# Optimization experiments

Measured on AMD Instinct MI355X. Metric: run time of the kernel, lower is better.

## Reference

```python
import jax, jax.numpy as jnp
import numpy as np

DIM = 128; HEADS = 8; HD = DIM // HEADS; RES = 32
HSP, WSP, SSP = 32, 4, 4  # idx=0 cross-shaped window
WIN = HSP * WSP * SSP
SCALE = HD ** -0.5


def setup_inputs() -> dict:
    key = jax.random.key(0)
    k1, k2, k3 = jax.random.split(key, 3)
    qkv = jax.random.normal(k1, (3, 2, RES ** 3, DIM), dtype=jnp.float32)
    w = jax.random.normal(k2, (DIM, 1, 5, 5, 5), dtype=jnp.float32) * 0.05
    b = jax.random.normal(k3, (DIM,), dtype=jnp.float32) * 0.05
    return {"qkv": qkv, "w": w, "b": b}


def _windows(x):
    B = x.shape[0]
    x = x.reshape(B, RES // HSP, HSP, RES // WSP, WSP, RES // SSP, SSP, DIM)
    x = x.transpose(0, 1, 3, 5, 2, 4, 6, 7)
    return x.reshape(-1, WIN, DIM)


def reference(qkv, w, b):
    q, k, v = qkv[0], qkv[1], qkv[2]  # each [B, L, C]
    B = q.shape[0]
    qw = _windows(q).reshape(-1, WIN, HEADS, HD).transpose(0, 2, 1, 3)
    kw = _windows(k).reshape(-1, WIN, HEADS, HD).transpose(0, 2, 1, 3)
    # v windows as [Bw, C, Hsp, Wsp, Ssp] for depthwise LePE conv
    vw = _windows(v).reshape(-1, HSP, WSP, SSP, DIM).transpose(0, 4, 1, 2, 3)
    lepe = jax.lax.conv_general_dilated(
        vw, w, (1, 1, 1), [(2, 2), (2, 2), (2, 2)],
        dimension_numbers=("NCDHW", "OIDHW", "NCDHW"),
        feature_group_count=DIM,
    ) + b[None, :, None, None, None]
    lepe = lepe.reshape(-1, HEADS, HD, WIN).transpose(0, 1, 3, 2)
    vh = vw.reshape(-1, HEADS, HD, WIN).transpose(0, 1, 3, 2)
    attn = jax.nn.softmax(jnp.einsum("bhqd,bhkd->bhqk", qw * SCALE, kw), axis=-1)
    x = jnp.einsum("bhqk,bhkd->bhqd", attn, vh) + lepe
    x = x.transpose(0, 2, 1, 3).reshape(-1, WIN, DIM)
    # windows2img
    x = x.reshape(B, RES // HSP, RES // WSP, RES // SSP, HSP, WSP, SSP, DIM)
    x = x.transpose(0, 1, 4, 2, 5, 3, 6, 7).reshape(B, RES ** 3, DIM)
    return x
```

## Files before the change

kernel.cpp:

```cpp
#include <hip/hip_runtime.h>
#include <stdint.h>

#define DIMC  128
#define HEADS 8
#define HD    16
#define WIN   512
#define LTOT  32768
#define NB    2

typedef __bf16 bf16x8_t __attribute__((ext_vector_type(8)));
typedef float f32x16_t  __attribute__((ext_vector_type(16)));
typedef float f32x4_t   __attribute__((ext_vector_type(4)));
typedef unsigned int u32x2_t __attribute__((ext_vector_type(2)));
union U128 { uint4 u; bf16x8_t v; };

__device__ __forceinline__ uint32_t rne_pair(float lo, float hi) {
    uint32_t a = __float_as_uint(lo), b = __float_as_uint(hi);
    a = (a + 0x7fffu + ((a >> 16) & 1u)) >> 16;
    b = (b + 0x7fffu + ((b >> 16) & 1u)) >> 16;
    return a | (b << 16);
}
__device__ __forceinline__ unsigned short rne1(float x) {
    uint32_t a = __float_as_uint(x);
    return (unsigned short)((a + 0x7fffu + ((a >> 16) & 1u)) >> 16);
}
__device__ __forceinline__ uint32_t trunc_pair(float lo, float hi) {
    return __builtin_amdgcn_perm(__float_as_uint(hi), __float_as_uint(lo), 0x07060302u);
}
__device__ __forceinline__ float fast_exp2(float x) {
#if __has_builtin(__builtin_amdgcn_exp2f)
    return __builtin_amdgcn_exp2f(x);
#else
    return exp2f(x);
#endif
}

__global__ void __launch_bounds__(256, 4) attn_lepe(
    const float* __restrict__ qkv,
    const float* __restrict__ wgt,
    const float* __restrict__ bias,
    float* __restrict__ out)
{
    __shared__ __align__(16) unsigned short Kf[16 * 512];
    __shared__ __align__(16) unsigned short Vt[17 * 520];
    __shared__ __align__(16) unsigned short Wb[125 * 16];
    __shared__ __align__(16) unsigned short Zp[16];

    const int blk  = blockIdx.x;
    const int head = blk >> 7;
    const int wi   = blk & 127;
    const int b    = wi >> 6;
    const int rem  = wi & 63;
    const int lbase = ((rem >> 3) << 7) + ((rem & 7) << 2);
    const int t    = threadIdx.x;
    const int lane = t & 63;
    const int wv   = t >> 6;
    const int cbase = head * HD;

    const int col  = lane & 31;
    const int hsel = lane >> 5;

    const float* Qg = qkv + (size_t)b * LTOT * DIMC;
    const float* Kg = Qg + (size_t)NB * LTOT * DIMC;
    const float* Vg = Kg + (size_t)NB * LTOT * DIMC;

    for (int u = t; u < 1024; u += 256) {
        int tp = u >> 2, ch4 = u & 3;
        int p  = tp << 1;
        int hh = p >> 4, ww = (p >> 2) & 3, ss = p & 3;
        int l  = (hh << 10) + lbase + (ww << 5) + ss;
        size_t g = (size_t)l * DIMC + cbase + (ch4 << 2);
        float4 k0 = *(const float4*)&Kg[g];
        float4 k1 = *(const float4*)&Kg[g + DIMC];
        float4 v0 = *(const float4*)&Vg[g];
        float4 v1 = *(const float4*)&Vg[g + DIMC];
        int c  = p >> 5;
        int fl = (p & 31) + ((ch4 >> 1) << 5);
        int jo = (ch4 & 1) << 2;
        *(uint2*)&Kf[c * 512 + fl * 8 + jo] =
            make_uint2(rne_pair(k0.x, k0.y), rne_pair(k0.z, k0.w));
        *(uint2*)&Kf[c * 512 + (fl + 1) * 8 + jo] =
            make_uint2(rne_pair(k1.x, k1.y), rne_pair(k1.z, k1.w));
        float a0[4] = {v0.x, v0.y, v0.z, v0.w};
        float a1[4] = {v1.x, v1.y, v1.z, v1.w};
#pragma unroll
        for (int i = 0; i < 4; ++i)
            *(uint32_t*)&Vt[((ch4 << 2) + i) * 520 + p] = rne_pair(a0[i], a1[i]);
    }
    if (t < 128) ((uint2*)&Vt[16 * 520])[t] = make_uint2(0x3F803F80u, 0x3F803F80u);
    if (t < 8)  ((uint32_t*)Zp)[t & 7] = 0u;
    for (int e = t; e < 125 * HD; e += 256) {
        int tap = e >> 4, d = e & 15;
        Wb[e] = rne1(wgt[(size_t)(cbase + d) * 125 + tap]);
    }

    const float QSC = 0.25f * 1.44269504088896340736f;
    bf16x8_t qf[4];
#pragma unroll
    for (int mt = 0; mt < 4; ++mt) {
        int qrow = wv * 128 + mt * 32 + col;
        int l = ((qrow >> 4) << 10) + lbase + (((qrow >> 2) & 3) << 5) + (qrow & 3);
        const float* qp = &Qg[(size_t)l * DIMC + cbase + hsel * 8];
        float4 a = *(const float4*)qp;
        float4 c4 = *(const float4*)(qp + 4);
        U128 u;
        u.u.x = rne_pair(a.x * QSC, a.y * QSC);
        u.u.y = rne_pair(a.z * QSC, a.w * QSC);
        u.u.z = rne_pair(c4.x * QSC, c4.y * QSC);
        u.u.w = rne_pair(c4.z * QSC, c4.w * QSC);
        qf[mt] = u.v;
    }
    float breg = (col < HD) ? bias[cbase + col] : 0.f;

    __syncthreads();

    f32x16_t acc[4];
#pragma unroll
    for (int mt = 0; mt < 4; ++mt)
#pragma unroll
        for (int i = 0; i < 16; ++i) acc[mt][i] = 0.f;
    f32x16_t zv;
#pragma unroll
    for (int i = 0; i < 16; ++i) zv[i] = 0.f;

    const int vcol = (col <= 16) ? col : 16;
    const int voff = vcol * 520;

    for (int c = 0; c < 16; ++c) {
        U128 kf;  kf.u  = *(const uint4*)&Kf[c * 512 + lane * 8];
        U128 vf0; vf0.u = *(const uint4*)&Vt[voff + c * 32 + hsel * 8];
        U128 vf1; vf1.u = *(const uint4*)&Vt[voff + c * 32 + 16 + hsel * 8];
#pragma unroll
        for (int mt = 0; mt < 4; ++mt) {
            f32x16_t S = __builtin_amdgcn_mfma_f32_32x32x16_bf16(kf.v, qf[mt], zv, 0, 0, 0);
            uint32_t pk[8];
#pragma unroll
            for (int r = 0; r < 8; ++r)
                pk[r] = trunc_pair(fast_exp2(S[2 * r]), fast_exp2(S[2 * r + 1]));
            U128 A0, A1;
#if __has_builtin(__builtin_amdgcn_permlane32_swap)
            u32x2_t rxz0 = __builtin_amdgcn_permlane32_swap(pk[0], pk[2], false, false);
            u32x2_t ryw0 = __builtin_amdgcn_permlane32_swap(pk[1], pk[3], false, false);
            u32x2_t rxz1 = __builtin_amdgcn_permlane32_swap(pk[4], pk[6], false, false);
            u32x2_t ryw1 = __builtin_amdgcn_permlane32_swap(pk[5], pk[7], false, false);
            A0.u = make_uint4(rxz0[0], ryw0[0], rxz0[1], ryw0[1]);
            A1.u = make_uint4(rxz1[0], ryw1[0], rxz1[1], ryw1[1]);
#else
            uint32_t xa = __shfl_xor(hsel ? pk[0] : pk[2], 32);
            uint32_t xb = __shfl_xor(hsel ? pk[1] : pk[3], 32);
            uint32_t xc = __shfl_xor(hsel ? pk[4] : pk[6], 32);
            uint32_t xd = __shfl_xor(hsel ? pk[5] : pk[7], 32);
            A0.u = hsel ? make_uint4(xa, xb, pk[2], pk[3])
                        : make_uint4(pk[0], pk[1], xa, xb);
            A1.u = hsel ? make_uint4(xc, xd, pk[6], pk[7])
                        : make_uint4(pk[4], pk[5], xc, xd);
#endif
            acc[mt] = __builtin_amdgcn_mfma_f32_32x32x16_bf16(A0.v, vf0.v, acc[mt], 0, 0, 0);
            acc[mt] = __builtin_amdgcn_mfma_f32_32x32x16_bf16(A1.v, vf1.v, acc[mt], 0, 0, 0);
        }
    }

    __syncthreads();

    {
        const int sg  = lane & 15;
        const int khi = lane >> 4;
        const int tb  = (khi & 1) * 8;
#pragma unroll
        for (int cc = 0; cc < 4; ++cc) {
            const int cch = wv * 4 + cc;
            U128 Bf[3];
#pragma unroll
            for (int kc = 0; kc < 3; ++kc) {
                int dh = 2 * kc + (khi >> 1);
                uint32_t pr[4];
#pragma unroll
                for (int jp = 0; jp < 4; ++jp) {
                    uint32_t w01 = 0;
#pragma unroll
                    for (int e = 0; e < 2; ++e) {
                        int tau = tb + jp * 2 + e;
                        int dw = (tau >> 2) - (sg >> 2);
                        int ds = (tau & 3) - (sg & 3);
                        bool valid = (dh < 5) && (dw >= -2) && (dw <= 2) && (ds >= -2) && (ds <= 2);
                        int tap = dh * 25 + (dw + 2) * 5 + (ds + 2);
                        uint32_t wv16 = valid ? (uint32_t)Wb[(valid ? tap : 0) * 16 + cch] : 0u;
                        w01 |= wv16 << (16 * e);
                    }
                    pr[jp] = w01;
                }
                Bf[kc].u = make_uint4(pr[0], pr[1], pr[2], pr[3]);
            }
#pragma unroll
            for (int mt2 = 0; mt2 < 2; ++mt2) {
                f32x4_t cacc = {0.f, 0.f, 0.f, 0.f};
#pragma unroll
                for (int kc = 0; kc < 3; ++kc) {
                    int dh = 2 * kc + (khi >> 1);
                    int h_in = mt2 * 16 + (lane & 15) + dh - 2;
                    const unsigned short* ap =
                        (h_in >= 0 && h_in < 32 && dh < 5)
                            ? &Vt[cch * 520 + h_in * 16 + tb]
                            : Zp;
                    U128 af; af.u = *(const uint4*)ap;
                    cacc = __builtin_amdgcn_mfma_f32_16x16x32_bf16(af.v, Bf[kc].v, cacc, 0, 0, 0);
                }
#pragma unroll
                for (int r = 0; r < 4; ++r) {
                    int h = mt2 * 16 + khi * 4 + r;
                    Kf[(h * 16 + sg) * 16 + cch] = rne1(cacc[r]);
                }
            }
        }
    }

    __syncthreads();

    const int ccol = col & 15;
#pragma unroll
    for (int mt = 0; mt < 4; ++mt) {
#pragma unroll
        for (int i = 0; i < 16; ++i) {
            float dv = __shfl(acc[mt][i], 16 | (lane & 32), 64);
            int row = (i & 3) + ((i >> 2) << 3) + (hsel << 2);
            int token = wv * 128 + mt * 32 + row;
            float cvv = __uint_as_float(((uint32_t)Kf[token * 16 + ccol]) << 16);
            float oval = acc[mt][i] * __builtin_amdgcn_rcpf(dv) + breg + cvv;
            if (col < HD) {
                int l = ((token >> 4) << 10) + lbase + (((token >> 2) & 3) << 5) + (token & 3);
                out[((size_t)b * LTOT + l) * DIMC + cbase + col] = oval;
            }
        }
    }
}

extern "C" void kernel_launch(void* const* d_in, const int* in_sizes, int n_in,
                              void* d_out, int out_size, void* d_ws, size_t ws_size,
                              hipStream_t stream) {
    const float* qkv  = (const float*)d_in[0];
    const float* wgt  = (const float*)d_in[1];
    const float* bias = (const float*)d_in[2];
    float* out = (float*)d_out;
    attn_lepe<<<dim3(1024), dim3(256), 0, stream>>>(qkv, wgt, bias, out);
}
```

Measured before the change: 195.8 us.

## Restructure attention loop into batched QK/exp phase then PV MFMA phase

The inner loop is reordered so each query tile first computes eight key-chunk score MFMAs and their exp/bf16 packing into a register array, then issues the sixteen PV MFMAs back to back under raised wave priority. This is meant to decouple the exp VALU work from dependent MFMA chains and let the scheduler overlap them across waves. Launch bounds drop from 4 to 2 blocks per CU to allow the larger register footprint, which lowers occupancy. It also reloads K and V fragments per query tile instead of once per chunk, adding LDS traffic.

After: 193.8 us. No clear change (-1.0%).

```diff
diff --git a/kernel.cpp b/kernel.cpp
--- a/kernel.cpp
+++ b/kernel.cpp
@@ -35,7 +35,7 @@
 #endif
 }
 
-__global__ void __launch_bounds__(256, 4) attn_lepe(
+__global__ void __launch_bounds__(256, 2) attn_lepe(
     const float* __restrict__ qkv,
     const float* __restrict__ wgt,
     const float* __restrict__ bias,
@@ -126,37 +126,57 @@
     const int vcol = (col <= 16) ? col : 16;
     const int voff = vcol * 520;
 
-    for (int c = 0; c < 16; ++c) {
-        U128 kf;  kf.u  = *(const uint4*)&Kf[c * 512 + lane * 8];
-        U128 vf0; vf0.u = *(const uint4*)&Vt[voff + c * 32 + hsel * 8];
-        U128 vf1; vf1.u = *(const uint4*)&Vt[voff + c * 32 + 16 + hsel * 8];
-#pragma unroll
-        for (int mt = 0; mt < 4; ++mt) {
-            f32x16_t S = __builtin_amdgcn_mfma_f32_32x32x16_bf16(kf.v, qf[mt], zv, 0, 0, 0);
-            uint32_t pk[8];
-#pragma unroll
-            for (int r = 0; r < 8; ++r)
-                pk[r] = trunc_pair(fast_exp2(S[2 * r]), fast_exp2(S[2 * r + 1]));
-            U128 A0, A1;
+#pragma unroll
+    for (int mt = 0; mt < 4; ++mt) {
+#pragma unroll
+        for (int half = 0; half < 2; ++half) {
+            uint32_t pa[8][8];
+
+#pragma unroll
+            for (int cc = 0; cc < 8; ++cc) {
+                const int c = half * 8 + cc;
+                U128 kf; kf.u = *(const uint4*)&Kf[c * 512 + lane * 8];
+                f32x16_t S = __builtin_amdgcn_mfma_f32_32x32x16_bf16(kf.v, qf[mt], zv, 0, 0, 0);
+                float pe[16];
+#pragma unroll
+                for (int r = 0; r < 16; ++r) pe[r] = fast_exp2(S[r]);
+                uint32_t pk[8];
+#pragma unroll
+                for (int r = 0; r < 8; ++r) pk[r] = trunc_pair(pe[2 * r], pe[2 * r + 1]);
 #if __has_builtin(__builtin_amdgcn_permlane32_swap)
-            u32x2_t rxz0 = __builtin_amdgcn_permlane32_swap(pk[0], pk[2], false, false);
-            u32x2_t ryw0 = __builtin_amdgcn_permlane32_swap(pk[1], pk[3], false, false);
-            u32x2_t rxz1 = __builtin_amdgcn_permlane32_swap(pk[4], pk[6], false, false);
-            u32x2_t ryw1 = __builtin_amdgcn_permlane32_swap(pk[5], pk[7], false, false);
-            A0.u = make_uint4(rxz0[0], ryw0[0], rxz0[1], ryw0[1]);
-            A1.u = make_uint4(rxz1[0], ryw1[0], rxz1[1], ryw1[1]);
+                u32x2_t rxz0 = __builtin_amdgcn_permlane32_swap(pk[0], pk[2], false, false);
+                u32x2_t ryw0 = __builtin_amdgcn_permlane32_swap(pk[1], pk[3], false, false);
+                u32x2_t rxz1 = __builtin_amdgcn_permlane32_swap(pk[4], pk[6], false, false);
+                u32x2_t ryw1 = __builtin_amdgcn_permlane32_swap(pk[5], pk[7], false, false);
+                pa[cc][0] = rxz0[0]; pa[cc][1] = ryw0[0];
+                pa[cc][2] = rxz0[1]; pa[cc][3] = ryw0[1];
+                pa[cc][4] = rxz1[0]; pa[cc][5] = ryw1[0];
+                pa[cc][6] = rxz1[1]; pa[cc][7] = ryw1[1];
 #else
-            uint32_t xa = __shfl_xor(hsel ? pk[0] : pk[2], 32);
-            uint32_t xb = __shfl_xor(hsel ? pk[1] : pk[3], 32);
-            uint32_t xc = __shfl_xor(hsel ? pk[4] : pk[6], 32);
-            uint32_t xd = __shfl_xor(hsel ? pk[5] : pk[7], 32);
-            A0.u = hsel ? make_uint4(xa, xb, pk[2], pk[3])
-                        : make_uint4(pk[0], pk[1], xa, xb);
-            A1.u = hsel ? make_uint4(xc, xd, pk[6], pk[7])
-                        : make_uint4(pk[4], pk[5], xc, xd);
+                uint32_t xa = __shfl_xor(hsel ? pk[0] : pk[2], 32);
+                uint32_t xb = __shfl_xor(hsel ? pk[1] : pk[3], 32);
+                uint32_t xc = __shfl_xor(hsel ? pk[4] : pk[6], 32);
+                uint32_t xd = __shfl_xor(hsel ? pk[5] : pk[7], 32);
+                pa[cc][0] = hsel ? xa : pk[0]; pa[cc][1] = hsel ? xb : pk[1];
+                pa[cc][2] = hsel ? pk[2] : xa; pa[cc][3] = hsel ? pk[3] : xb;
+                pa[cc][4] = hsel ? xc : pk[4]; pa[cc][5] = hsel ? xd : pk[5];
+                pa[cc][6] = hsel ? pk[6] : xc; pa[cc][7] = hsel ? pk[7] : xd;
 #endif
-            acc[mt] = __builtin_amdgcn_mfma_f32_32x32x16_bf16(A0.v, vf0.v, acc[mt], 0, 0, 0);
-            acc[mt] = __builtin_amdgcn_mfma_f32_32x32x16_bf16(A1.v, vf1.v, acc[mt], 0, 0, 0);
+            }
+
+            __builtin_amdgcn_s_setprio(1);
+#pragma unroll
+            for (int cc = 0; cc < 8; ++cc) {
+                const int c = half * 8 + cc;
+                U128 vf0; vf0.u = *(const uint4*)&Vt[voff + c * 32 + hsel * 8];
+                U128 vf1; vf1.u = *(const uint4*)&Vt[voff + c * 32 + 16 + hsel * 8];
+                U128 A0, A1;
+                A0.u = make_uint4(pa[cc][0], pa[cc][1], pa[cc][2], pa[cc][3]);
+                A1.u = make_uint4(pa[cc][4], pa[cc][5], pa[cc][6], pa[cc][7]);
+                acc[mt] = __builtin_amdgcn_mfma_f32_32x32x16_bf16(A0.v, vf0.v, acc[mt], 0, 0, 0);
+                acc[mt] = __builtin_amdgcn_mfma_f32_32x32x16_bf16(A1.v, vf1.v, acc[mt], 0, 0, 0);
+            }
+            __builtin_amdgcn_s_setprio(0);
         }
     }
 
```
